# Optimization experiments

Hardware: AMD Instinct MI355X
Metric: run time of the kernel (lower is better)

The kernel has to match this reference:

```python
import jax, jax.numpy as jnp
import numpy as np

B, M, SV, OV, R, L, V, E = 256, 10, 32, 32, 128, 12, 1000, 64
M2 = M * M
STATE_DIM = (SV + 1) * M2  # 3300
OBJ_DIM = OV * M2          # 3200


def setup_inputs() -> dict:
    key = jax.random.key(0)
    ks = jax.random.split(key, 24)
    s = 0.02
    inp = {
        "state": jax.random.randint(ks[0], (B, M2), 0, SV),
        "obj": jax.random.randint(ks[1], (B, M2), 0, OV),
        "text": jax.random.randint(ks[2], (B, L), 0, V),
        # state MLP [STATE_DIM,128,128,R]
        "Ws1": jax.random.normal(ks[3], (STATE_DIM, 128)) * s,
        "bs1": jnp.zeros((128,)),
        "Ws2": jax.random.normal(ks[4], (128, 128)) * s,
        "bs2": jnp.zeros((128,)),
        "Ws3": jax.random.normal(ks[5], (128, R)) * s,
        "bs3": jnp.zeros((R,)),
        # object MLP [OBJ_DIM,128,128,R]
        "Wo1": jax.random.normal(ks[6], (OBJ_DIM, 128)) * s,
        "bo1": jnp.zeros((128,)),
        "Wo2": jax.random.normal(ks[7], (128, 128)) * s,
        "bo2": jnp.zeros((128,)),
        "Wo3": jax.random.normal(ks[8], (128, R)) * s,
        "bo3": jnp.zeros((R,)),
        # LSTM text encoder: embedding + single-layer LSTM with hidden=R
        "emb": jax.random.normal(ks[9], (V, E)) * s,
        "Wih": jax.random.normal(ks[10], (E, 4 * R)) * s,
        "Whh": jax.random.normal(ks[11], (R, 4 * R)) * s,
        "b_lstm": jnp.zeros((4 * R,)),
    }
    return inp


def _mlp(x, W1, b1, W2, b2, W3, b3):
    h = jax.nn.relu(x @ W1 + b1)
    h = jax.nn.relu(h @ W2 + b2)
    return h @ W3 + b3


def _lstm_last_hidden(text, emb, Wih, Whh, b):
    # text: (B, L) ids -> final hidden (B, R)
    x = emb[text]                      # (B, L, E)
    xs = jnp.swapaxes(x, 0, 1)         # (L, B, E)
    h0 = jnp.zeros((text.shape[0], R), x.dtype)
    c0 = jnp.zeros((text.shape[0], R), x.dtype)

    def step(carry, xt):
        h, c = carry
        g = xt @ Wih + h @ Whh + b     # (B, 4R)
        i, f, gg, o = jnp.split(g, 4, axis=-1)
        c = jax.nn.sigmoid(f) * c + jax.nn.sigmoid(i) * jnp.tanh(gg)
        h = jax.nn.sigmoid(o) * jnp.tanh(c)
        return (h, c), None

    (h, _), _ = jax.lax.scan(step, (h0, c0), xs)
    return h


def reference(state, obj, text, Ws1, bs1, Ws2, bs2, Ws3, bs3,
              Wo1, bo1, Wo2, bo2, Wo3, bo3, emb, Wih, Whh, b_lstm):
    b = state.shape[0]
    # one-hot encodings (torch scatter_ over channel dim)
    state_oh = jax.nn.one_hot(state, SV, dtype=jnp.float32)   # (B, 100, SV)
    obj_oh = jax.nn.one_hot(obj, OV, dtype=jnp.float32)       # (B, 100, OV)

    # repeat each map map_dim^2 times; copy p gets a one-hot of agent position p
    pos = jnp.eye(M2, dtype=jnp.float32)[None, :, :, None]    # (1, 100 copies, 100 cells, 1)
    state_rep = jnp.broadcast_to(state_oh[:, None], (b, M2, M2, SV))
    state_inp = jnp.concatenate(
        [state_rep, jnp.broadcast_to(pos, (b, M2, M2, 1))], axis=-1
    ).reshape(b * M2, STATE_DIM)
    obj_inp = jnp.broadcast_to(obj_oh[:, None], (b, M2, M2, OV)).reshape(b * M2, OBJ_DIM)

    state_out = _mlp(state_inp, Ws1, bs1, Ws2, bs2, Ws3, bs3)   # (B*100, R)
    object_out = _mlp(obj_inp, Wo1, bo1, Wo2, bo2, Wo3, bo3)    # (B*100, R)

    # text is identical across the 100 copies -> encode once, broadcast
    h = _lstm_last_hidden(text, emb, Wih, Whh, b_lstm)          # (B, R)
    lstm_out = jnp.broadcast_to(h[:, None], (b, M2, R)).reshape(b * M2, R)

    values = state_out * object_out * lstm_out                 # (B*100, R)
    map_pred = values.sum(1).reshape(b, M, M)
    return map_pred
```

## Files before the change

### kernel.cpp

```cpp
#include <hip/hip_runtime.h>


#define B_   256
#define M2_  100
#define R_   128
#define L_   12
#define E_   64
#define NT   1024

typedef _Float16 half2v __attribute__((ext_vector_type(2)));
typedef _Float16 f16x8  __attribute__((ext_vector_type(8)));
typedef float    f32x4  __attribute__((ext_vector_type(4)));

__device__ __forceinline__ float sigf(float x) { return 1.f / (1.f + expf(-x)); }

__device__ __forceinline__ uint pk16(float a, float b) {
    half2v h; h.x = (_Float16)a; h.y = (_Float16)b;
    return __builtin_bit_cast(uint, h);
}

__global__ __launch_bounds__(NT, 4) void uvfa_kernel(
    const int* __restrict__ state, const int* __restrict__ obj, const int* __restrict__ text,
    const float* __restrict__ Ws1, const float* __restrict__ bs1,
    const float* __restrict__ Ws2, const float* __restrict__ bs2,
    const float* __restrict__ Ws3, const float* __restrict__ bs3,
    const float* __restrict__ Wo1, const float* __restrict__ bo1,
    const float* __restrict__ Wo2, const float* __restrict__ bo2,
    const float* __restrict__ Wo3, const float* __restrict__ bo3,
    const float* __restrict__ emb, const float* __restrict__ Wih,
    const float* __restrict__ Whh, const float* __restrict__ b_lstm,
    float* __restrict__ out)
{
    const int b   = blockIdx.x;
    const int tid = threadIdx.x;

    __shared__ __align__(16) uint  U[15840];
    __shared__ __align__(16) float part[NT];
    __shared__ __align__(16) float hbuf[R_];
    __shared__ __align__(16) uint  hpair[R_ / 2];
    __shared__ __align__(16) float tmp[R_], tmp2[R_], wbuf[R_], ubuf[R_], bsbuf[R_];
    __shared__ float redw2[2][112];
    __shared__ int   idx_o[M2_], idx_s[M2_], tids[L_];
    __shared__ float c0s;

    float* xw   = (float*)U;
    float* xemb = (float*)(U + 8192);

    const int lane = tid & 63;
    const int wv   = tid >> 6;
    const int m16  = lane & 15;
    const int kgrp = lane >> 4;

    f16x8 af[2][4];
    #pragma unroll
    for (int tt = 0; tt < 2; ++tt) {
        int col = (2 * wv + tt) * 16 + m16;
        #pragma unroll
        for (int s = 0; s < 4; ++s) {
            int kb = s * 32 + kgrp * 8;
            #pragma unroll
            for (int e = 0; e < 8; ++e)
                af[tt][s][e] = (_Float16)Whh[(kb + e) * 512 + col];
        }
    }

    if (tid < M2_) idx_o[tid] = obj[b * M2_ + tid];
    else if (tid >= 128 && tid < 128 + M2_) idx_s[tid - 128] = state[b * M2_ + tid - 128];
    else if (tid >= 256 && tid < 256 + L_) tids[tid - 256] = text[b * L_ + tid - 256];
    else if (tid >= 384 && tid < 448) hpair[tid - 384] = 0u;
    __syncthreads();
    if (tid < L_ * E_) xemb[(tid >> 6) * 66 + (tid & 63)] = emb[tids[tid >> 6] * E_ + (tid & 63)];
    else if (tid < L_ * E_ + 264) ((float*)(U + 8192 + 792))[tid - L_ * E_] = 0.f;
    __syncthreads();

    {
        f16x8 ax[2];
        #pragma unroll
        for (int s = 0; s < 2; ++s) {
            #pragma unroll
            for (int e = 0; e < 8; ++e)
                ax[s][e] = (_Float16)xemb[m16 * 66 + s * 32 + kgrp * 8 + e];
        }
        #pragma unroll
        for (int h = 0; h < 2; ++h) {
            int col = (wv * 2 + h) * 16 + m16;
            float bl = b_lstm[col];
            f32x4 acc = { bl, bl, bl, bl };
            #pragma unroll
            for (int s = 0; s < 2; ++s) {
                f16x8 bx;
                #pragma unroll
                for (int e = 0; e < 8; ++e)
                    bx[e] = (_Float16)Wih[(s * 32 + kgrp * 8 + e) * 512 + col];
                acc = __builtin_amdgcn_mfma_f32_16x16x32_f16(ax[s], bx, acc, 0, 0, 0);
            }
            if (kgrp < 3) {
                #pragma unroll
                for (int r = 0; r < 4; ++r)
                    xw[(kgrp * 4 + r) * 512 + col] = acc[r];
            }
        }
    }
    __syncthreads();

    float cst = 0.f;
    for (int t = 0; t < L_; ++t) {
        f16x8 bf[4];
        #pragma unroll
        for (int s = 0; s < 4; ++s) {
            uint4 hb = *(const uint4*)&hpair[s * 16 + kgrp * 4];
            bf[s] = __builtin_bit_cast(f16x8, hb);
        }
        #pragma unroll
        for (int tt = 0; tt < 2; ++tt) {
            int colb = (2 * wv + tt) * 16 + kgrp * 4;
            f32x4 acc = *(const f32x4*)&xw[t * 512 + colb];
            #pragma unroll
            for (int s = 0; s < 4; ++s)
                acc = __builtin_amdgcn_mfma_f32_16x16x32_f16(af[tt][s], bf[s], acc, 0, 0, 0);
            if (m16 == 0) {
                part[colb + 0] = acc[0];
                part[colb + 1] = acc[1];
                part[colb + 2] = acc[2];
                part[colb + 3] = acc[3];
            }
        }
        __syncthreads();
        if (tid < R_) {
            float gi = part[tid], gf = part[R_ + tid], gg = part[2 * R_ + tid], go = part[3 * R_ + tid];
            cst = sigf(gf) * cst + sigf(gi) * tanhf(gg);
            float hn = sigf(go) * tanhf(cst);
            hbuf[tid] = hn;
            float hs = __shfl_down(hn, 1, 64);
            if (!(tid & 1)) hpair[tid >> 1] = pk16(hn, hs);
        }
        __syncthreads();
    }

    #pragma unroll
    for (int idx = tid; idx < 64 * 128; idx += NT) {
        int jp = idx >> 7, kk = idx & 127;
        U[jp * 132 + kk] = pk16(Ws2[(2 * jp) * R_ + kk], Ws2[(2 * jp + 1) * R_ + kk]);
    }

    const int k = tid & 127, qq = tid >> 7;
    {
        float acc = 0.f;
        int c0i = qq * 13, c1i = c0i + 13 < M2_ ? c0i + 13 : M2_;
        for (int c = c0i; c < c1i; ++c)
            acc += Wo1[(c * 32 + idx_o[c]) * R_ + k];
        part[qq * R_ + k] = acc;
    }
    __syncthreads();
    if (tid < R_) {
        float a = bo1[tid];
        #pragma unroll
        for (int q8 = 0; q8 < 8; ++q8) a += part[q8 * R_ + tid];
        tmp[tid] = fmaxf(a, 0.f);
    }
    __syncthreads();
    {
        float s0 = 0.f, s1 = 0.f, s2 = 0.f, s3 = 0.f;
        int j0 = qq * 16;
        #pragma unroll
        for (int j = 0; j < 16; j += 4) {
            s0 = fmaf(tmp[j0 + j + 0], Wo2[(j0 + j + 0) * R_ + k], s0);
            s1 = fmaf(tmp[j0 + j + 1], Wo2[(j0 + j + 1) * R_ + k], s1);
            s2 = fmaf(tmp[j0 + j + 2], Wo2[(j0 + j + 2) * R_ + k], s2);
            s3 = fmaf(tmp[j0 + j + 3], Wo2[(j0 + j + 3) * R_ + k], s3);
        }
        part[qq * R_ + k] = (s0 + s1) + (s2 + s3);
    }
    __syncthreads();
    if (tid < R_) {
        float a = bo2[tid];
        #pragma unroll
        for (int q8 = 0; q8 < 8; ++q8) a += part[q8 * R_ + tid];
        tmp2[tid] = fmaxf(a, 0.f);
    }
    __syncthreads();
    {
        float s0 = 0.f, s1 = 0.f, s2 = 0.f, s3 = 0.f;
        int j0 = qq * 16;
        #pragma unroll
        for (int j = 0; j < 16; j += 4) {
            s0 = fmaf(tmp2[j0 + j + 0], Wo3[(j0 + j + 0) * R_ + k], s0);
            s1 = fmaf(tmp2[j0 + j + 1], Wo3[(j0 + j + 1) * R_ + k], s1);
            s2 = fmaf(tmp2[j0 + j + 2], Wo3[(j0 + j + 2) * R_ + k], s2);
            s3 = fmaf(tmp2[j0 + j + 3], Wo3[(j0 + j + 3) * R_ + k], s3);
        }
        part[qq * R_ + k] = (s0 + s1) + (s2 + s3);
    }
    __syncthreads();
    if (tid < R_) {
        float a = bo3[tid];
        #pragma unroll
        for (int q8 = 0; q8 < 8; ++q8) a += part[q8 * R_ + tid];
        wbuf[tid] = a * hbuf[tid];
    }
    __syncthreads();

    {
        float s0 = 0.f, s1 = 0.f, s2 = 0.f, s3 = 0.f;
        int j0 = qq * 16;
        const float4* w3 = reinterpret_cast<const float4*>(&Ws3[k * R_ + j0]);
        #pragma unroll
        for (int jj = 0; jj < 4; ++jj) {
            float4 v = w3[jj];
            s0 = fmaf(v.x, wbuf[j0 + jj * 4 + 0], s0);
            s1 = fmaf(v.y, wbuf[j0 + jj * 4 + 1], s1);
            s2 = fmaf(v.z, wbuf[j0 + jj * 4 + 2], s2);
            s3 = fmaf(v.w, wbuf[j0 + jj * 4 + 3], s3);
        }
        part[qq * R_ + k] = (s0 + s1) + (s2 + s3);
    }
    if (tid >= 960) {
        int j = tid - 960;
        float s = bs3[j] * wbuf[j] + bs3[j + 64] * wbuf[j + 64];
        s += __shfl_down(s, 32, 64);
        s += __shfl_down(s, 16, 64);
        s += __shfl_down(s, 8, 64);
        s += __shfl_down(s, 4, 64);
        s += __shfl_down(s, 2, 64);
        s += __shfl_down(s, 1, 64);
        if (j == 0) c0s = s;
    }
    __syncthreads();
    if (tid < R_) {
        float a = 0.f;
        #pragma unroll
        for (int q8 = 0; q8 < 8; ++q8) a += part[q8 * R_ + tid];
        ubuf[tid] = a;
    }
    __syncthreads();

    {
        float acc = 0.f;
        int c0i = qq * 13, c1i = c0i + 13 < M2_ ? c0i + 13 : M2_;
        for (int c = c0i; c < c1i; ++c)
            acc += Ws1[(c * 33 + idx_s[c]) * R_ + k];
        part[qq * R_ + k] = acc;
    }
    __syncthreads();
    if (tid < R_) {
        float a = bs1[tid];
        #pragma unroll
        for (int q8 = 0; q8 < 8; ++q8) a += part[q8 * R_ + tid];
        bsbuf[tid] = a;
    }
    __syncthreads();

    #pragma unroll 4
    for (int pass = 0; pass < 13; ++pass) {
        int idx = pass * NT + tid;
        if (idx < M2_ * R_) {
            int j = idx & 127, p = idx >> 7;
            float v = fmaxf(bsbuf[j] + Ws1[(p * 33 + 32) * R_ + j], 0.f);
            float v2 = __shfl_down(v, 1, 64);
            if (!(j & 1)) U[8448 + p * 66 + (j >> 1)] = pk16(v, v2);
        }
    }
    if (tid < 792) U[8448 + 6600 + tid] = 0u;
    __syncthreads();

    if (wv < 14) {
        const int mtile = wv >> 1, nhalf = wv & 1;
        const uint* Ap = U + 8448 + (mtile * 16 + m16) * 66;
        f16x8 A[4];
        #pragma unroll
        for (int s = 0; s < 4; ++s) {
            int jb = s * 16 + kgrp * 4;
            uint4 av = { Ap[jb + 0], Ap[jb + 1], Ap[jb + 2], Ap[jb + 3] };
            A[s] = __builtin_bit_cast(f16x8, av);
        }
        f32x4 acc[4] = { {0,0,0,0}, {0,0,0,0}, {0,0,0,0}, {0,0,0,0} };
        #pragma unroll
        for (int nt = 0; nt < 4; ++nt) {
            int ko = (nhalf * 4 + nt) * 16 + m16;
            #pragma unroll
            for (int s = 0; s < 4; ++s) {
                const uint* Bp = U + (s * 16 + kgrp * 4) * 132 + ko;
                uint4 bv = { Bp[0], Bp[132], Bp[264], Bp[396] };
                acc[nt] = __builtin_amdgcn_mfma_f32_16x16x32_f16(
                    A[s], __builtin_bit_cast(f16x8, bv), acc[nt], 0, 0, 0);
            }
        }
        float vs0 = 0.f, vs1 = 0.f, vs2 = 0.f, vs3 = 0.f;
        #pragma unroll
        for (int nt = 0; nt < 4; ++nt) {
            int ko = (nhalf * 4 + nt) * 16 + m16;
            float bb = bs2[ko], uu = ubuf[ko];
            vs0 = fmaf(fmaxf(acc[nt][0] + bb, 0.f), uu, vs0);
            vs1 = fmaf(fmaxf(acc[nt][1] + bb, 0.f), uu, vs1);
            vs2 = fmaf(fmaxf(acc[nt][2] + bb, 0.f), uu, vs2);
            vs3 = fmaf(fmaxf(acc[nt][3] + bb, 0.f), uu, vs3);
        }
        vs0 += __shfl_xor(vs0, 1, 64); vs0 += __shfl_xor(vs0, 2, 64);
        vs0 += __shfl_xor(vs0, 4, 64); vs0 += __shfl_xor(vs0, 8, 64);
        vs1 += __shfl_xor(vs1, 1, 64); vs1 += __shfl_xor(vs1, 2, 64);
        vs1 += __shfl_xor(vs1, 4, 64); vs1 += __shfl_xor(vs1, 8, 64);
        vs2 += __shfl_xor(vs2, 1, 64); vs2 += __shfl_xor(vs2, 2, 64);
        vs2 += __shfl_xor(vs2, 4, 64); vs2 += __shfl_xor(vs2, 8, 64);
        vs3 += __shfl_xor(vs3, 1, 64); vs3 += __shfl_xor(vs3, 2, 64);
        vs3 += __shfl_xor(vs3, 4, 64); vs3 += __shfl_xor(vs3, 8, 64);
        if (m16 == 0) {
            int pr = mtile * 16 + kgrp * 4;
            redw2[nhalf][pr + 0] = vs0;
            redw2[nhalf][pr + 1] = vs1;
            redw2[nhalf][pr + 2] = vs2;
            redw2[nhalf][pr + 3] = vs3;
        }
    }
    __syncthreads();

    if (tid < M2_)
        out[b * M2_ + tid] = c0s + redw2[0][tid] + redw2[1][tid];
}

extern "C" void kernel_launch(void* const* d_in, const int* in_sizes, int n_in,
                              void* d_out, int out_size, void* d_ws, size_t ws_size,
                              hipStream_t stream) {
    const int*   state  = (const int*)d_in[0];
    const int*   obj    = (const int*)d_in[1];
    const int*   text   = (const int*)d_in[2];
    const float* Ws1    = (const float*)d_in[3];
    const float* bs1    = (const float*)d_in[4];
    const float* Ws2    = (const float*)d_in[5];
    const float* bs2    = (const float*)d_in[6];
    const float* Ws3    = (const float*)d_in[7];
    const float* bs3    = (const float*)d_in[8];
    const float* Wo1    = (const float*)d_in[9];
    const float* bo1    = (const float*)d_in[10];
    const float* Wo2    = (const float*)d_in[11];
    const float* bo2    = (const float*)d_in[12];
    const float* Wo3    = (const float*)d_in[13];
    const float* bo3    = (const float*)d_in[14];
    const float* emb    = (const float*)d_in[15];
    const float* Wih    = (const float*)d_in[16];
    const float* Whh    = (const float*)d_in[17];
    const float* b_lstm = (const float*)d_in[18];
    float* out = (float*)d_out;

    hipLaunchKernelGGL(uvfa_kernel, dim3(B_), dim3(NT), 0, stream,
                       state, obj, text, Ws1, bs1, Ws2, bs2, Ws3, bs3,
                       Wo1, bo1, Wo2, bo2, Wo3, bo3, emb, Wih, Whh, b_lstm, out);
}
```

Measured before the change: 39.34 us.

## Prepack LSTM and Ws2 weights to fp16 in a separate kernel for vector loads

```diff
diff --git a/kernel.cpp b/kernel.cpp
--- a/kernel.cpp
+++ b/kernel.cpp
@@ -19,22 +19,45 @@
     return __builtin_bit_cast(uint, h);
 }
 
-__global__ __launch_bounds__(NT, 4) void uvfa_kernel(
+__global__ __launch_bounds__(256) void pack_kernel(
+    const float* __restrict__ Whh, const float* __restrict__ Wih,
+    const float* __restrict__ Ws2, void* __restrict__ wsv)
+{
+    _Float16* WhhT = (_Float16*)wsv;
+    _Float16* WihT = WhhT + 65536;
+    uint*     W2P  = (uint*)(WihT + 32768);
+    int g = blockIdx.x * 256 + threadIdx.x;
+    if (g < 65536) {
+        int r = g >> 9, c = g & 511;
+        WhhT[c * 128 + r] = (_Float16)Whh[r * 512 + c];
+    } else if (g < 65536 + 32768) {
+        int g2 = g - 65536;
+        int e = g2 >> 9, c = g2 & 511;
+        WihT[c * 64 + e] = (_Float16)Wih[e * 512 + c];
+    } else if (g < 65536 + 32768 + 8192) {
+        int g3 = g - 65536 - 32768;
+        int jp = g3 >> 7, kk = g3 & 127;
+        W2P[g3] = pk16(Ws2[(2 * jp) * R_ + kk], Ws2[(2 * jp + 1) * R_ + kk]);
+    }
+}
+
+__global__ __launch_bounds__(NT) __attribute__((amdgpu_waves_per_eu(4, 4)))
+void uvfa_kernel(
     const int* __restrict__ state, const int* __restrict__ obj, const int* __restrict__ text,
     const float* __restrict__ Ws1, const float* __restrict__ bs1,
-    const float* __restrict__ Ws2, const float* __restrict__ bs2,
-    const float* __restrict__ Ws3, const float* __restrict__ bs3,
+    const float* __restrict__ bs2, const float* __restrict__ Ws3, const float* __restrict__ bs3,
     const float* __restrict__ Wo1, const float* __restrict__ bo1,
     const float* __restrict__ Wo2, const float* __restrict__ bo2,
     const float* __restrict__ Wo3, const float* __restrict__ bo3,
-    const float* __restrict__ emb, const float* __restrict__ Wih,
-    const float* __restrict__ Whh, const float* __restrict__ b_lstm,
+    const float* __restrict__ emb, const float* __restrict__ b_lstm,
+    const _Float16* __restrict__ WhhT, const _Float16* __restrict__ WihT,
+    const uint* __restrict__ W2P,
     float* __restrict__ out)
 {
     const int b   = blockIdx.x;
     const int tid = threadIdx.x;
 
-    __shared__ __align__(16) uint  U[15840];
+    __shared__ __align__(16) uint  U[16064];
     __shared__ __align__(16) float part[NT];
     __shared__ __align__(16) float hbuf[R_];
     __shared__ __align__(16) uint  hpair[R_ / 2];
@@ -56,12 +79,8 @@
     for (int tt = 0; tt < 2; ++tt) {
         int col = (2 * wv + tt) * 16 + m16;
         #pragma unroll
-        for (int s = 0; s < 4; ++s) {
-            int kb = s * 32 + kgrp * 8;
-            #pragma unroll
-            for (int e = 0; e < 8; ++e)
-                af[tt][s][e] = (_Float16)Whh[(kb + e) * 512 + col];
-        }
+        for (int s = 0; s < 4; ++s)
+            af[tt][s] = *(const f16x8*)&WhhT[col * 128 + s * 32 + kgrp * 8];
     }
 
     if (tid < M2_) idx_o[tid] = obj[b * M2_ + tid];
@@ -88,10 +107,7 @@
             f32x4 acc = { bl, bl, bl, bl };
             #pragma unroll
             for (int s = 0; s < 2; ++s) {
-                f16x8 bx;
-                #pragma unroll
-                for (int e = 0; e < 8; ++e)
-                    bx[e] = (_Float16)Wih[(s * 32 + kgrp * 8 + e) * 512 + col];
+                f16x8 bx = *(const f16x8*)&WihT[col * 64 + s * 32 + kgrp * 8];
                 acc = __builtin_amdgcn_mfma_f32_16x16x32_f16(ax[s], bx, acc, 0, 0, 0);
             }
             if (kgrp < 3) {
@@ -137,10 +153,14 @@
         __syncthreads();
     }
 
-    #pragma unroll
-    for (int idx = tid; idx < 64 * 128; idx += NT) {
-        int jp = idx >> 7, kk = idx & 127;
-        U[jp * 132 + kk] = pk16(Ws2[(2 * jp) * R_ + kk], Ws2[(2 * jp + 1) * R_ + kk]);
+    {
+        const uint4* src = (const uint4*)W2P;
+        #pragma unroll
+        for (int idx = tid; idx < 2048; idx += NT) {
+            uint4 v = src[idx];
+            int jp = idx >> 5, kq = idx & 31;
+            *(uint4*)&U[jp * 132 + kq * 4] = v;
+        }
     }
 
     const int k = tid & 127, qq = tid >> 7;
@@ -257,22 +277,19 @@
             int j = idx & 127, p = idx >> 7;
             float v = fmaxf(bsbuf[j] + Ws1[(p * 33 + 32) * R_ + j], 0.f);
             float v2 = __shfl_down(v, 1, 64);
-            if (!(j & 1)) U[8448 + p * 66 + (j >> 1)] = pk16(v, v2);
-        }
-    }
-    if (tid < 792) U[8448 + 6600 + tid] = 0u;
+            if (!(j & 1)) U[8448 + p * 68 + (j >> 1)] = pk16(v, v2);
+        }
+    }
+    if (tid < 816) U[8448 + 6800 + tid] = 0u;
     __syncthreads();
 
     if (wv < 14) {
         const int mtile = wv >> 1, nhalf = wv & 1;
-        const uint* Ap = U + 8448 + (mtile * 16 + m16) * 66;
+        const uint* Ap = U + 8448 + (mtile * 16 + m16) * 68;
         f16x8 A[4];
         #pragma unroll
-        for (int s = 0; s < 4; ++s) {
-            int jb = s * 16 + kgrp * 4;
-            uint4 av = { Ap[jb + 0], Ap[jb + 1], Ap[jb + 2], Ap[jb + 3] };
-            A[s] = __builtin_bit_cast(f16x8, av);
-        }
+        for (int s = 0; s < 4; ++s)
+            A[s] = __builtin_bit_cast(f16x8, *(const uint4*)&Ap[s * 16 + kgrp * 4]);
         f32x4 acc[4] = { {0,0,0,0}, {0,0,0,0}, {0,0,0,0}, {0,0,0,0} };
         #pragma unroll
         for (int nt = 0; nt < 4; ++nt) {
@@ -341,7 +358,13 @@
     const float* b_lstm = (const float*)d_in[18];
     float* out = (float*)d_out;
 
+    _Float16* WhhT = (_Float16*)d_ws;
+    _Float16* WihT = WhhT + 65536;
+    uint*     W2P  = (uint*)(WihT + 32768);
+
+    hipLaunchKernelGGL(pack_kernel, dim3(416), dim3(256), 0, stream, Whh, Wih, Ws2, d_ws);
     hipLaunchKernelGGL(uvfa_kernel, dim3(B_), dim3(NT), 0, stream,
-                       state, obj, text, Ws1, bs1, Ws2, bs2, Ws3, bs3,
-                       Wo1, bo1, Wo2, bo2, Wo3, bo3, emb, Wih, Whh, b_lstm, out);
+                       state, obj, text, Ws1, bs1, bs2, Ws3, bs3,
+                       Wo1, bo1, Wo2, bo2, Wo3, bo3, emb, b_lstm,
+                       WhhT, WihT, W2P, out);
 }
```

Result: no change. 39.85 us (+1.3%).

## Fuse LSTM gate math into MFMA waves with double-buffered hidden state

Applied to the files above, without the earlier changes.

```diff
diff --git a/kernel.cpp b/kernel.cpp
--- a/kernel.cpp
+++ b/kernel.cpp
@@ -12,12 +12,15 @@
 typedef _Float16 f16x8  __attribute__((ext_vector_type(8)));
 typedef float    f32x4  __attribute__((ext_vector_type(4)));
 
-__device__ __forceinline__ float sigf(float x) { return 1.f / (1.f + expf(-x)); }
+__device__ __forceinline__ float sigf(float x)   { return 1.f / (1.f + __expf(-x)); }
+__device__ __forceinline__ float tanhff(float x) { float e = __expf(-2.f * x); return (1.f - e) / (1.f + e); }
 
 __device__ __forceinline__ uint pk16(float a, float b) {
     half2v h; h.x = (_Float16)a; h.y = (_Float16)b;
     return __builtin_bit_cast(uint, h);
 }
+
+#define PINU4(v) asm volatile("" : "+v"(v.x), "+v"(v.y), "+v"(v.z), "+v"(v.w));
 
 __global__ __launch_bounds__(NT, 4) void uvfa_kernel(
     const int* __restrict__ state, const int* __restrict__ obj, const int* __restrict__ text,
@@ -34,10 +37,10 @@
     const int b   = blockIdx.x;
     const int tid = threadIdx.x;
 
-    __shared__ __align__(16) uint  U[15840];
+    __shared__ __align__(16) uint  U[16064];
     __shared__ __align__(16) float part[NT];
     __shared__ __align__(16) float hbuf[R_];
-    __shared__ __align__(16) uint  hpair[R_ / 2];
+    __shared__ __align__(16) uint  hpair[2][64];
     __shared__ __align__(16) float tmp[R_], tmp2[R_], wbuf[R_], ubuf[R_], bsbuf[R_];
     __shared__ float redw2[2][112];
     __shared__ int   idx_o[M2_], idx_s[M2_], tids[L_];
@@ -50,24 +53,30 @@
     const int wv   = tid >> 6;
     const int m16  = lane & 15;
     const int kgrp = lane >> 4;
-
-    f16x8 af[2][4];
-    #pragma unroll
-    for (int tt = 0; tt < 2; ++tt) {
-        int col = (2 * wv + tt) * 16 + m16;
-        #pragma unroll
-        for (int s = 0; s < 4; ++s) {
-            int kb = s * 32 + kgrp * 8;
-            #pragma unroll
-            for (int e = 0; e < 8; ++e)
-                af[tt][s][e] = (_Float16)Whh[(kb + e) * 512 + col];
+    const int k = tid & 127, qq = tid >> 7;
+
+    uint4 afu[4][4];
+    if (wv < 8) {
+        #pragma unroll
+        for (int g = 0; g < 4; ++g) {
+            int col = (wv + 8 * g) * 16 + m16;
+            #pragma unroll
+            for (int s = 0; s < 4; ++s) {
+                f16x8 t;
+                int kb = s * 32 + kgrp * 8;
+                #pragma unroll
+                for (int e = 0; e < 8; ++e)
+                    t[e] = (_Float16)Whh[(kb + e) * 512 + col];
+                afu[g][s] = __builtin_bit_cast(uint4, t);
+                PINU4(afu[g][s])
+            }
         }
     }
 
     if (tid < M2_) idx_o[tid] = obj[b * M2_ + tid];
     else if (tid >= 128 && tid < 128 + M2_) idx_s[tid - 128] = state[b * M2_ + tid - 128];
     else if (tid >= 256 && tid < 256 + L_) tids[tid - 256] = text[b * L_ + tid - 256];
-    else if (tid >= 384 && tid < 448) hpair[tid - 384] = 0u;
+    else if (tid >= 384 && tid < 448) hpair[0][tid - 384] = 0u;
     __syncthreads();
     if (tid < L_ * E_) xemb[(tid >> 6) * 66 + (tid & 63)] = emb[tids[tid >> 6] * E_ + (tid & 63)];
     else if (tid < L_ * E_ + 264) ((float*)(U + 8192 + 792))[tid - L_ * E_] = 0.f;
@@ -103,38 +112,46 @@
     }
     __syncthreads();
 
-    float cst = 0.f;
+    float cst0 = 0.f, cst1 = 0.f, cst2 = 0.f, cst3 = 0.f;
+    float h0 = 0.f, h1v = 0.f, h2v = 0.f, h3v = 0.f;
     for (int t = 0; t < L_; ++t) {
-        f16x8 bf[4];
-        #pragma unroll
-        for (int s = 0; s < 4; ++s) {
-            uint4 hb = *(const uint4*)&hpair[s * 16 + kgrp * 4];
-            bf[s] = __builtin_bit_cast(f16x8, hb);
-        }
-        #pragma unroll
-        for (int tt = 0; tt < 2; ++tt) {
-            int colb = (2 * wv + tt) * 16 + kgrp * 4;
-            f32x4 acc = *(const f32x4*)&xw[t * 512 + colb];
+        if (wv < 8) {
+            const uint* hp = hpair[t & 1];
+            f16x8 bf[4];
             #pragma unroll
             for (int s = 0; s < 4; ++s)
-                acc = __builtin_amdgcn_mfma_f32_16x16x32_f16(af[tt][s], bf[s], acc, 0, 0, 0);
+                bf[s] = __builtin_bit_cast(f16x8, *(const uint4*)&hp[s * 16 + kgrp * 4]);
+            f32x4 acc[4];
+            #pragma unroll
+            for (int g = 0; g < 4; ++g) {
+                acc[g] = *(const f32x4*)&xw[t * 512 + (wv + 8 * g) * 16 + kgrp * 4];
+                #pragma unroll
+                for (int s = 0; s < 4; ++s)
+                    acc[g] = __builtin_amdgcn_mfma_f32_16x16x32_f16(
+                        __builtin_bit_cast(f16x8, afu[g][s]), bf[s], acc[g], 0, 0, 0);
+            }
+            cst0 = sigf(acc[1][0]) * cst0 + sigf(acc[0][0]) * tanhff(acc[2][0]);
+            h0   = sigf(acc[3][0]) * tanhff(cst0);
+            cst1 = sigf(acc[1][1]) * cst1 + sigf(acc[0][1]) * tanhff(acc[2][1]);
+            h1v  = sigf(acc[3][1]) * tanhff(cst1);
+            cst2 = sigf(acc[1][2]) * cst2 + sigf(acc[0][2]) * tanhff(acc[2][2]);
+            h2v  = sigf(acc[3][2]) * tanhff(cst2);
+            cst3 = sigf(acc[1][3]) * cst3 + sigf(acc[0][3]) * tanhff(acc[2][3]);
+            h3v  = sigf(acc[3][3]) * tanhff(cst3);
             if (m16 == 0) {
-                part[colb + 0] = acc[0];
-                part[colb + 1] = acc[1];
-                part[colb + 2] = acc[2];
-                part[colb + 3] = acc[3];
+                uint* hw = hpair[(t + 1) & 1];
+                hw[8 * wv + kgrp * 2]     = pk16(h0, h1v);
+                hw[8 * wv + kgrp * 2 + 1] = pk16(h2v, h3v);
             }
         }
         __syncthreads();
-        if (tid < R_) {
-            float gi = part[tid], gf = part[R_ + tid], gg = part[2 * R_ + tid], go = part[3 * R_ + tid];
-            cst = sigf(gf) * cst + sigf(gi) * tanhf(gg);
-            float hn = sigf(go) * tanhf(cst);
-            hbuf[tid] = hn;
-            float hs = __shfl_down(hn, 1, 64);
-            if (!(tid & 1)) hpair[tid >> 1] = pk16(hn, hs);
-        }
-        __syncthreads();
+    }
+    if (wv < 8 && m16 == 0) {
+        int j = wv * 16 + kgrp * 4;
+        hbuf[j + 0] = h0;
+        hbuf[j + 1] = h1v;
+        hbuf[j + 2] = h2v;
+        hbuf[j + 3] = h3v;
     }
 
     #pragma unroll
@@ -143,7 +160,6 @@
         U[jp * 132 + kk] = pk16(Ws2[(2 * jp) * R_ + kk], Ws2[(2 * jp + 1) * R_ + kk]);
     }
 
-    const int k = tid & 127, qq = tid >> 7;
     {
         float acc = 0.f;
         int c0i = qq * 13, c1i = c0i + 13 < M2_ ? c0i + 13 : M2_;
@@ -257,22 +273,19 @@
             int j = idx & 127, p = idx >> 7;
             float v = fmaxf(bsbuf[j] + Ws1[(p * 33 + 32) * R_ + j], 0.f);
             float v2 = __shfl_down(v, 1, 64);
-            if (!(j & 1)) U[8448 + p * 66 + (j >> 1)] = pk16(v, v2);
-        }
-    }
-    if (tid < 792) U[8448 + 6600 + tid] = 0u;
+            if (!(j & 1)) U[8448 + p * 68 + (j >> 1)] = pk16(v, v2);
+        }
+    }
+    if (tid < 816) U[8448 + 6800 + tid] = 0u;
     __syncthreads();
 
     if (wv < 14) {
         const int mtile = wv >> 1, nhalf = wv & 1;
-        const uint* Ap = U + 8448 + (mtile * 16 + m16) * 66;
+        const uint* Ap = U + 8448 + (mtile * 16 + m16) * 68;
         f16x8 A[4];
         #pragma unroll
-        for (int s = 0; s < 4; ++s) {
-            int jb = s * 16 + kgrp * 4;
-            uint4 av = { Ap[jb + 0], Ap[jb + 1], Ap[jb + 2], Ap[jb + 3] };
-            A[s] = __builtin_bit_cast(f16x8, av);
-        }
+        for (int s = 0; s < 4; ++s)
+            A[s] = __builtin_bit_cast(f16x8, *(const uint4*)&Ap[s * 16 + kgrp * 4]);
         f32x4 acc[4] = { {0,0,0,0}, {0,0,0,0}, {0,0,0,0}, {0,0,0,0} };
         #pragma unroll
         for (int nt = 0; nt < 4; ++nt) {
```

Result: slower. 41.53 us (+5.6%).
